# Kernel optimization log

Measured on AMD Instinct MI355X. Metric: run time of the kernel, lower is better.

## Reference

```python
import jax, jax.numpy as jnp
import numpy as np

N_HEAD = 12
HEAD_SIZE = 64
HIDDEN = N_HEAD * HEAD_SIZE  # 768


def setup_inputs() -> dict:
    key = jax.random.key(0)
    k1, k2, k3 = jax.random.split(key, 3)
    B, S = 2, 2048
    hidden_states = jax.random.normal(k1, (B, S, HIDDEN), dtype=jnp.float32)
    c_attn_w = jax.random.normal(k2, (HIDDEN, 3 * HIDDEN), dtype=jnp.float32) * 0.02
    c_attn_b = jnp.zeros((3 * HIDDEN,), dtype=jnp.float32)
    c_proj_w = jax.random.normal(k3, (HIDDEN, HIDDEN), dtype=jnp.float32) * 0.02
    c_proj_b = jnp.zeros((HIDDEN,), dtype=jnp.float32)
    return {
        "hidden_states": hidden_states,
        "c_attn_w": c_attn_w,
        "c_attn_b": c_attn_b,
        "c_proj_w": c_proj_w,
        "c_proj_b": c_proj_b,
    }


def reference(hidden_states, c_attn_w, c_attn_b, c_proj_w, c_proj_b):
    B, S, H = hidden_states.shape
    scale = 1.0 / (HEAD_SIZE ** 0.5)
    # QKV projection (Conv1D: x @ W + b)
    qkv = hidden_states @ c_attn_w + c_attn_b  # [B, S, 3H]
    q, k, v = jnp.split(qkv, 3, axis=-1)
    # [B, n_head, S, head_size]
    def split_heads(t):
        return t.reshape(B, S, N_HEAD, HEAD_SIZE).transpose(0, 2, 1, 3)
    q, k, v = split_heads(q), split_heads(k), split_heads(v)
    # scores: [B, n_head, S, S]
    scores = jnp.einsum("bhqd,bhkd->bhqk", q, k) * scale
    mask_value = jnp.finfo(hidden_states.dtype).min
    causal = jnp.triu(jnp.full((S, S), mask_value, dtype=hidden_states.dtype), k=1)
    scores = scores + causal
    weights = jax.nn.softmax(scores, axis=-1)
    ctx = jnp.einsum("bhqk,bhkd->bhqd", weights, v)  # [B, n_head, S, head_size]
    ctx = ctx.transpose(0, 2, 1, 3).reshape(B, S, H)
    out = ctx @ c_proj_w + c_proj_b
    return out
```

## Files before the change

kernel.cpp:

```cpp
#include <hip/hip_runtime.h>

typedef __bf16 bf16x8 __attribute__((ext_vector_type(8)));
typedef __bf16 bf16x4 __attribute__((ext_vector_type(4)));
typedef float  f32x4  __attribute__((ext_vector_type(4)));

#define N_HEAD 12
#define HEAD   64
#define HID    768
#define SEQ    2048
#define BATCH  2
#define BH     (BATCH*N_HEAD)
#define MROWS  (BATCH*SEQ)
#define VSTR   2080
#define SC2    0.18033688011112042f

static __device__ __forceinline__ f32x4 mfma32(bf16x8 a, bf16x8 b, f32x4 c) {
    return __builtin_amdgcn_mfma_f32_16x16x32_bf16(a, b, c, 0, 0, 0);
}

#define GLOAD_LDS16(gp, lp) __builtin_amdgcn_global_load_lds( \
    (const __attribute__((address_space(1))) void*)(gp), \
    (__attribute__((address_space(3))) void*)(lp), 16, 0, 0)

__global__ __launch_bounds__(256) void cast_f32_bf16(const float* __restrict__ in,
                                                     __bf16* __restrict__ out, int n8) {
    int i = blockIdx.x * 256 + threadIdx.x;
    if (i >= n8) return;
    const float4* p = (const float4*)in;
    float4 a = p[2*i], b = p[2*i+1];
    bf16x8 o;
    o[0]=(__bf16)a.x; o[1]=(__bf16)a.y; o[2]=(__bf16)a.z; o[3]=(__bf16)a.w;
    o[4]=(__bf16)b.x; o[5]=(__bf16)b.y; o[6]=(__bf16)b.z; o[7]=(__bf16)b.w;
    *(bf16x8*)&out[(size_t)8*i] = o;
}

__global__ __launch_bounds__(256) void transpose_cast(const float* __restrict__ in,
                                                      __bf16* __restrict__ out, int R, int C) {
    __shared__ float t[32][33];
    int bx = blockIdx.x * 32;
    int by = blockIdx.y * 32;
    int x = threadIdx.x, y = threadIdx.y;
    #pragma unroll
    for (int i = 0; i < 32; i += 8) t[y+i][x] = in[(size_t)(by+y+i)*C + bx + x];
    __syncthreads();
    #pragma unroll
    for (int i = 0; i < 32; i += 8) out[(size_t)(bx+y+i)*R + by + x] = (__bf16)t[x][y+i];
}

template<int EPI>
__global__ __launch_bounds__(256) void gemm_bt(
    const __bf16* __restrict__ A, const __bf16* __restrict__ Bt,
    const float* __restrict__ bias, float* __restrict__ Cout,
    __bf16* __restrict__ Qo, __bf16* __restrict__ Ko, __bf16* __restrict__ Vo,
    int M, int N, int K)
{
    __shared__ __align__(16) __bf16 As[128*64];
    __shared__ __align__(16) __bf16 Bs[128*64];
    int tid = threadIdx.x;
    int m0 = blockIdx.y * 128, n0 = blockIdx.x * 128;
    int wave = tid >> 6, lane = tid & 63, lr = lane & 15, lk = lane >> 4;
    int wr = wave >> 1, wc = wave & 1;

    f32x4 acc[4][4];
    f32x4 zz = {0.f, 0.f, 0.f, 0.f};
    #pragma unroll
    for (int m = 0; m < 4; m++)
        #pragma unroll
        for (int n = 0; n < 4; n++) acc[m][n] = zz;

    for (int k0 = 0; k0 < K; k0 += 64) {
        #pragma unroll
        for (int i = 0; i < 4; i++) {
            int u = tid + 256*i;
            int row = u >> 3;
            int c = (u & 7) ^ (row & 7);
            GLOAD_LDS16(&A [(size_t)(m0+row)*K + k0 + c*8], &As[(size_t)u*8]);
            GLOAD_LDS16(&Bt[(size_t)(n0+row)*K + k0 + c*8], &Bs[(size_t)u*8]);
        }
        __syncthreads();
        #pragma unroll
        for (int kk = 0; kk < 2; kk++) {
            bf16x8 af[4], bfr[4];
            #pragma unroll
            for (int m = 0; m < 4; m++) {
                int row = wr*64 + m*16 + lr;
                int byte = (row*128 + kk*64 + lk*16) ^ ((row & 7) << 4);
                af[m] = *(const bf16x8*)((const char*)As + byte);
            }
            #pragma unroll
            for (int n = 0; n < 4; n++) {
                int row = wc*64 + n*16 + lr;
                int byte = (row*128 + kk*64 + lk*16) ^ ((row & 7) << 4);
                bfr[n] = *(const bf16x8*)((const char*)Bs + byte);
            }
            #pragma unroll
            for (int m = 0; m < 4; m++)
                #pragma unroll
                for (int n = 0; n < 4; n++)
                    acc[m][n] = mfma32(af[m], bfr[n], acc[m][n]);
        }
        __syncthreads();
    }

    #pragma unroll
    for (int m = 0; m < 4; m++)
    #pragma unroll
    for (int n = 0; n < 4; n++)
    #pragma unroll
    for (int r = 0; r < 4; r++) {
        int row = m0 + wr*64 + m*16 + lk*4 + r;
        int col = n0 + wc*64 + n*16 + lr;
        float v = acc[m][n][r] + bias[col];
        if (EPI == 0) {
            Cout[(size_t)row * N + col] = v;
        } else {
            int b_idx = row >> 11, s = row & 2047;
            int which = col / HID, hc = col % HID;
            int bh = b_idx * N_HEAD + (hc >> 6);
            int d = hc & 63;
            if (which == 0)      Qo[((size_t)bh*SEQ + s)*HEAD + d] = (__bf16)(v * SC2);
            else if (which == 1) Ko[((size_t)bh*SEQ + s)*HEAD + d] = (__bf16)v;
            else                 Vo[((size_t)bh*HEAD + d)*VSTR + s] = (__bf16)v;
        }
    }
}

__global__ __launch_bounds__(256, 2) void flash_attn(
    const __bf16* __restrict__ Q, const __bf16* __restrict__ Km,
    const __bf16* __restrict__ Vt, __bf16* __restrict__ ctx)
{
    __shared__ __align__(16) __bf16 Ks[2][64*64];
    __shared__ __align__(16) __bf16 Vs[2][64*64];
    int tid = threadIdx.x;
    int w = tid >> 6;
    int lane = tid & 63;
    int lr = lane & 15, lk = lane >> 4;
    int gid = blockIdx.x;
    int bh = gid % BH;
    int qb = 15 - gid / BH;
    int b_idx = bh / N_HEAD, h = bh % N_HEAD;
    int q0 = qb*128 + w*32;
    const size_t hb = (size_t)bh * SEQ * HEAD;
    const size_t vbh = (size_t)bh * HEAD * VSTR;
    f32x4 zz = {0.f, 0.f, 0.f, 0.f};

    int u0 = tid, u1 = tid + 256;
    int kr0 = u0 >> 3, kc0 = (u0 & 7) ^ (kr0 & 7);
    int kr1 = u1 >> 3, kc1 = (u1 & 7) ^ (kr1 & 7);

    bf16x8 qf0[2], qf1[2];
    #pragma unroll
    for (int kb = 0; kb < 2; kb++) {
        qf0[kb] = *(const bf16x8*)&Q[hb + (size_t)(q0 + lr)*HEAD + kb*32 + lk*8];
        qf1[kb] = *(const bf16x8*)&Q[hb + (size_t)(q0 + 16 + lr)*HEAD + kb*32 + lk*8];
    }

    f32x4 acc0[4], acc1[4];
    float ls0 = 0.f, ls1 = 0.f;
    #pragma unroll
    for (int db = 0; db < 4; db++) { acc0[db] = zz; acc1[db] = zz; }

    int nt = 2*qb + 2;

    GLOAD_LDS16(&Km[hb + (size_t)kr0*HEAD + kc0*8],  &Ks[0][(size_t)u0*8]);
    GLOAD_LDS16(&Km[hb + (size_t)kr1*HEAD + kc1*8],  &Ks[0][(size_t)u1*8]);
    GLOAD_LDS16(&Vt[vbh + (size_t)kr0*VSTR + kc0*8], &Vs[0][(size_t)u0*8]);
    GLOAD_LDS16(&Vt[vbh + (size_t)kr1*VSTR + kc1*8], &Vs[0][(size_t)u1*8]);
    __syncthreads();

    for (int t = 0; t < nt; t++) {
        int kv0 = t * 64;
        int cur = t & 1;
        const char* kbuf = (const char*)&Ks[cur][0];
        const char* vbuf = (const char*)&Vs[cur][0];

        if (t + 1 < nt) {
            int kv1 = kv0 + 64;
            int nxt = cur ^ 1;
            GLOAD_LDS16(&Km[hb + (size_t)(kv1 + kr0)*HEAD + kc0*8],  &Ks[nxt][(size_t)u0*8]);
            GLOAD_LDS16(&Km[hb + (size_t)(kv1 + kr1)*HEAD + kc1*8],  &Ks[nxt][(size_t)u1*8]);
            GLOAD_LDS16(&Vt[vbh + (size_t)kr0*VSTR + kv1 + kc0*8],   &Vs[nxt][(size_t)u0*8]);
            GLOAD_LDS16(&Vt[vbh + (size_t)kr1*VSTR + kv1 + kc1*8],   &Vs[nxt][(size_t)u1*8]);
        }

        bf16x8 kf[4][2];
        #pragma unroll
        for (int cb = 0; cb < 4; cb++)
            #pragma unroll
            for (int kb = 0; kb < 2; kb++) {
                int row = cb*16 + lr;
                int byte = (row*128 + kb*64 + lk*16) ^ ((row & 7) << 4);
                kf[cb][kb] = *(const bf16x8*)(kbuf + byte);
            }

        bf16x8 v01[4], v23[4];
        #pragma unroll
        for (int db = 0; db < 4; db++) {
            int row = db*16 + lr;
            int rx = (row & 7) << 4;
            bf16x4 a0 = *(const bf16x4*)(vbuf + ((row*128 + lk*8)       ^ rx));
            bf16x4 a1 = *(const bf16x4*)(vbuf + ((row*128 + 32 + lk*8)  ^ rx));
            bf16x4 a2 = *(const bf16x4*)(vbuf + ((row*128 + 64 + lk*8)  ^ rx));
            bf16x4 a3 = *(const bf16x4*)(vbuf + ((row*128 + 96 + lk*8)  ^ rx));
            v01[db] = __builtin_shufflevector(a0, a1, 0,1,2,3,4,5,6,7);
            v23[db] = __builtin_shufflevector(a2, a3, 0,1,2,3,4,5,6,7);
        }

        f32x4 sc0[4], sc1[4];
        __builtin_amdgcn_s_setprio(1);
        #pragma unroll
        for (int cb = 0; cb < 4; cb++) {
            f32x4 z0 = mfma32(kf[cb][0], qf0[0], zz);
            sc0[cb] = mfma32(kf[cb][1], qf0[1], z0);
            f32x4 z1 = mfma32(kf[cb][0], qf1[0], zz);
            sc1[cb] = mfma32(kf[cb][1], qf1[1], z1);
        }
        __builtin_amdgcn_s_setprio(0);

        if (kv0 + 63 > q0) {
            #pragma unroll
            for (int cb = 0; cb < 4; cb++)
                #pragma unroll
                for (int r = 0; r < 4; r++) {
                    int kg = kv0 + cb*16 + lk*4 + r;
                    if (kg > q0 + lr)      sc0[cb][r] = -30000.f;
                    if (kg > q0 + 16 + lr) sc1[cb][r] = -30000.f;
                }
        }

        bf16x8 pa0[2], pa1[2];
        {
            float rs0 = 0.f, rs1 = 0.f;
            #pragma unroll
            for (int cb = 0; cb < 4; cb++)
                #pragma unroll
                for (int r = 0; r < 4; r++) {
                    float p0 = exp2f(sc0[cb][r]);
                    float p1 = exp2f(sc1[cb][r]);
                    rs0 += p0; rs1 += p1;
                    pa0[cb >> 1][(cb & 1)*4 + r] = (__bf16)p0;
                    pa1[cb >> 1][(cb & 1)*4 + r] = (__bf16)p1;
                }
            ls0 += rs0; ls1 += rs1;
        }

        __builtin_amdgcn_s_setprio(1);
        #pragma unroll
        for (int db = 0; db < 4; db++) {
            acc0[db] = mfma32(pa0[0], v01[db], acc0[db]);
            acc0[db] = mfma32(pa0[1], v23[db], acc0[db]);
            acc1[db] = mfma32(pa1[0], v01[db], acc1[db]);
            acc1[db] = mfma32(pa1[1], v23[db], acc1[db]);
        }
        __builtin_amdgcn_s_setprio(0);

        __syncthreads();
    }

    float rs0 = ls0;
    rs0 += __shfl_xor(rs0, 16);
    rs0 += __shfl_xor(rs0, 32);
    float rs1 = ls1;
    rs1 += __shfl_xor(rs1, 16);
    rs1 += __shfl_xor(rs1, 32);
    float rl0 = 1.0f / rs0, rl1 = 1.0f / rs1;
    float li0[4], li1[4];
    #pragma unroll
    for (int r = 0; r < 4; r++) {
        li0[r] = __shfl(rl0, (lane & 48) | (lk*4 + r));
        li1[r] = __shfl(rl1, (lane & 48) | (lk*4 + r));
    }

    #pragma unroll
    for (int db = 0; db < 4; db++)
        #pragma unroll
        for (int r = 0; r < 4; r++) {
            int d = db*16 + lr;
            int qg0 = q0 + lk*4 + r;
            int qg1 = q0 + 16 + lk*4 + r;
            ctx[((size_t)(b_idx*SEQ + qg0))*HID + h*HEAD + d] = (__bf16)(acc0[db][r] * li0[r]);
            ctx[((size_t)(b_idx*SEQ + qg1))*HID + h*HEAD + d] = (__bf16)(acc1[db][r] * li1[r]);
        }
}

extern "C" void kernel_launch(void* const* d_in, const int* in_sizes, int n_in,
                              void* d_out, int out_size, void* d_ws, size_t ws_size,
                              hipStream_t stream) {
    const float* x  = (const float*)d_in[0];
    const float* w1 = (const float*)d_in[1];
    const float* b1 = (const float*)d_in[2];
    const float* w2 = (const float*)d_in[3];
    const float* b2 = (const float*)d_in[4];
    float* out = (float*)d_out;

    char* ws = (char*)d_ws;
    size_t o = 0;
    __bf16* Xb  = (__bf16*)(ws + o); o += (size_t)MROWS*HID*2;
    __bf16* W1t = (__bf16*)(ws + o); o += (size_t)3*HID*HID*2;
    __bf16* W2t = (__bf16*)(ws + o); o += (size_t)HID*HID*2;
    __bf16* Qb  = (__bf16*)(ws + o); o += (size_t)MROWS*HID*2;
    __bf16* Kb  = (__bf16*)(ws + o); o += (size_t)MROWS*HID*2;
    __bf16* Vt  = (__bf16*)(ws + o); o += (size_t)BH*HEAD*VSTR*2;
    __bf16* CTX = (__bf16*)(ws + o); o += (size_t)MROWS*HID*2;

    cast_f32_bf16<<<(MROWS*HID/8 + 255)/256, 256, 0, stream>>>(x, Xb, MROWS*HID/8);
    transpose_cast<<<dim3(3*HID/32, HID/32), dim3(32, 8), 0, stream>>>(w1, W1t, HID, 3*HID);
    transpose_cast<<<dim3(HID/32,   HID/32), dim3(32, 8), 0, stream>>>(w2, W2t, HID, HID);

    gemm_bt<1><<<dim3(3*HID/128, MROWS/128), 256, 0, stream>>>(
        Xb, W1t, b1, nullptr, Qb, Kb, Vt, MROWS, 3*HID, HID);

    flash_attn<<<dim3(16*BH), 256, 0, stream>>>(Qb, Kb, Vt, CTX);

    gemm_bt<0><<<dim3(HID/128, MROWS/128), 256, 0, stream>>>(
        CTX, W2t, b2, out, nullptr, nullptr, nullptr, MROWS, HID, HID);
}
```

Before: 189.2 us.

## Split long causal query blocks across two KV halves and double-buffer GEMM tiles

The attention kernel now splits each of the upper eight query blocks across two workgroups that process alternating KV tiles. Each writes unnormalized partial outputs and row sums into reused workspace, and a new combine kernel merges them and normalizes. This balances the causal triangle's uneven work across more workgroups. Separately, the projection GEMM gains a double-buffered LDS prefetch of the next K tile, so loads overlap with MFMA work. The cost is an extra kernel launch, extra global traffic for the partials, and twice the GEMM LDS footprint, which may lower occupancy.

```diff
diff --git a/kernel.cpp b/kernel.cpp
--- a/kernel.cpp
+++ b/kernel.cpp
@@ -54,13 +54,21 @@
     __bf16* __restrict__ Qo, __bf16* __restrict__ Ko, __bf16* __restrict__ Vo,
     int M, int N, int K)
 {
-    __shared__ __align__(16) __bf16 As[128*64];
-    __shared__ __align__(16) __bf16 Bs[128*64];
+    __shared__ __align__(16) __bf16 As[2][128*64];
+    __shared__ __align__(16) __bf16 Bs[2][128*64];
     int tid = threadIdx.x;
     int m0 = blockIdx.y * 128, n0 = blockIdx.x * 128;
     int wave = tid >> 6, lane = tid & 63, lr = lane & 15, lk = lane >> 4;
     int wr = wave >> 1, wc = wave & 1;
 
+    int ur[4], uc[4];
+    #pragma unroll
+    for (int i = 0; i < 4; i++) {
+        int u = tid + 256*i;
+        ur[i] = u >> 3;
+        uc[i] = (u & 7) ^ (ur[i] & 7);
+    }
+
     f32x4 acc[4][4];
     f32x4 zz = {0.f, 0.f, 0.f, 0.f};
     #pragma unroll
@@ -68,16 +76,29 @@
         #pragma unroll
         for (int n = 0; n < 4; n++) acc[m][n] = zz;
 
-    for (int k0 = 0; k0 < K; k0 += 64) {
-        #pragma unroll
-        for (int i = 0; i < 4; i++) {
-            int u = tid + 256*i;
-            int row = u >> 3;
-            int c = (u & 7) ^ (row & 7);
-            GLOAD_LDS16(&A [(size_t)(m0+row)*K + k0 + c*8], &As[(size_t)u*8]);
-            GLOAD_LDS16(&Bt[(size_t)(n0+row)*K + k0 + c*8], &Bs[(size_t)u*8]);
-        }
-        __syncthreads();
+    const int NK = K >> 6;
+    #pragma unroll
+    for (int i = 0; i < 4; i++) {
+        int u = tid + 256*i;
+        GLOAD_LDS16(&A [(size_t)(m0+ur[i])*K + uc[i]*8], &As[0][(size_t)u*8]);
+        GLOAD_LDS16(&Bt[(size_t)(n0+ur[i])*K + uc[i]*8], &Bs[0][(size_t)u*8]);
+    }
+    __syncthreads();
+
+    for (int ki = 0; ki < NK; ki++) {
+        int cur = ki & 1;
+        if (ki + 1 < NK) {
+            int k1 = (ki + 1) << 6;
+            int nxt = cur ^ 1;
+            #pragma unroll
+            for (int i = 0; i < 4; i++) {
+                int u = tid + 256*i;
+                GLOAD_LDS16(&A [(size_t)(m0+ur[i])*K + k1 + uc[i]*8], &As[nxt][(size_t)u*8]);
+                GLOAD_LDS16(&Bt[(size_t)(n0+ur[i])*K + k1 + uc[i]*8], &Bs[nxt][(size_t)u*8]);
+            }
+        }
+        const char* ab = (const char*)&As[cur][0];
+        const char* bb = (const char*)&Bs[cur][0];
         #pragma unroll
         for (int kk = 0; kk < 2; kk++) {
             bf16x8 af[4], bfr[4];
@@ -85,13 +106,13 @@
             for (int m = 0; m < 4; m++) {
                 int row = wr*64 + m*16 + lr;
                 int byte = (row*128 + kk*64 + lk*16) ^ ((row & 7) << 4);
-                af[m] = *(const bf16x8*)((const char*)As + byte);
+                af[m] = *(const bf16x8*)(ab + byte);
             }
             #pragma unroll
             for (int n = 0; n < 4; n++) {
                 int row = wc*64 + n*16 + lr;
                 int byte = (row*128 + kk*64 + lk*16) ^ ((row & 7) << 4);
-                bfr[n] = *(const bf16x8*)((const char*)Bs + byte);
+                bfr[n] = *(const bf16x8*)(bb + byte);
             }
             #pragma unroll
             for (int m = 0; m < 4; m++)
@@ -127,7 +148,8 @@
 
 __global__ __launch_bounds__(256, 2) void flash_attn(
     const __bf16* __restrict__ Q, const __bf16* __restrict__ Km,
-    const __bf16* __restrict__ Vt, __bf16* __restrict__ ctx)
+    const __bf16* __restrict__ Vt, __bf16* __restrict__ ctx,
+    __bf16* __restrict__ Opart, float* __restrict__ lspart)
 {
     __shared__ __align__(16) __bf16 Ks[2][64*64];
     __shared__ __align__(16) __bf16 Vs[2][64*64];
@@ -136,8 +158,19 @@
     int lane = tid & 63;
     int lr = lane & 15, lk = lane >> 4;
     int gid = blockIdx.x;
-    int bh = gid % BH;
-    int qb = 15 - gid / BH;
+    int bh, qb, half, step;
+    if (gid < 16*BH) {
+        qb = 15 - gid / (2*BH);
+        half = (gid % (2*BH)) / BH;
+        bh = gid % BH;
+        step = 2;
+    } else {
+        int u = gid - 16*BH;
+        qb = 7 - u / BH;
+        bh = u % BH;
+        half = 0; step = 1;
+    }
+    bool split = (step == 2);
     int b_idx = bh / N_HEAD, h = bh % N_HEAD;
     int q0 = qb*128 + w*32;
     const size_t hb = (size_t)bh * SEQ * HEAD;
@@ -161,22 +194,26 @@
     for (int db = 0; db < 4; db++) { acc0[db] = zz; acc1[db] = zz; }
 
     int nt = 2*qb + 2;
-
-    GLOAD_LDS16(&Km[hb + (size_t)kr0*HEAD + kc0*8],  &Ks[0][(size_t)u0*8]);
-    GLOAD_LDS16(&Km[hb + (size_t)kr1*HEAD + kc1*8],  &Ks[0][(size_t)u1*8]);
-    GLOAD_LDS16(&Vt[vbh + (size_t)kr0*VSTR + kc0*8], &Vs[0][(size_t)u0*8]);
-    GLOAD_LDS16(&Vt[vbh + (size_t)kr1*VSTR + kc1*8], &Vs[0][(size_t)u1*8]);
+    int t0 = half;
+
+    {
+        int kv = t0 * 64;
+        GLOAD_LDS16(&Km[hb + (size_t)(kv+kr0)*HEAD + kc0*8],  &Ks[0][(size_t)u0*8]);
+        GLOAD_LDS16(&Km[hb + (size_t)(kv+kr1)*HEAD + kc1*8],  &Ks[0][(size_t)u1*8]);
+        GLOAD_LDS16(&Vt[vbh + (size_t)kr0*VSTR + kv + kc0*8], &Vs[0][(size_t)u0*8]);
+        GLOAD_LDS16(&Vt[vbh + (size_t)kr1*VSTR + kv + kc1*8], &Vs[0][(size_t)u1*8]);
+    }
     __syncthreads();
 
-    for (int t = 0; t < nt; t++) {
+    int buf = 0;
+    for (int t = t0; t < nt; t += step) {
         int kv0 = t * 64;
-        int cur = t & 1;
-        const char* kbuf = (const char*)&Ks[cur][0];
-        const char* vbuf = (const char*)&Vs[cur][0];
-
-        if (t + 1 < nt) {
-            int kv1 = kv0 + 64;
-            int nxt = cur ^ 1;
+        const char* kbuf = (const char*)&Ks[buf][0];
+        const char* vbuf = (const char*)&Vs[buf][0];
+
+        if (t + step < nt) {
+            int kv1 = (t + step) * 64;
+            int nxt = buf ^ 1;
             GLOAD_LDS16(&Km[hb + (size_t)(kv1 + kr0)*HEAD + kc0*8],  &Ks[nxt][(size_t)u0*8]);
             GLOAD_LDS16(&Km[hb + (size_t)(kv1 + kr1)*HEAD + kc1*8],  &Ks[nxt][(size_t)u1*8]);
             GLOAD_LDS16(&Vt[vbh + (size_t)kr0*VSTR + kv1 + kc0*8],   &Vs[nxt][(size_t)u0*8]);
@@ -255,6 +292,7 @@
         __builtin_amdgcn_s_setprio(0);
 
         __syncthreads();
+        buf ^= 1;
     }
 
     float rs0 = ls0;
@@ -263,6 +301,26 @@
     float rs1 = ls1;
     rs1 += __shfl_xor(rs1, 16);
     rs1 += __shfl_xor(rs1, 32);
+
+    if (split) {
+        size_t ob = ((size_t)half*BH + bh) * 1024;
+        #pragma unroll
+        for (int db = 0; db < 4; db++)
+            #pragma unroll
+            for (int r = 0; r < 4; r++) {
+                int d = db*16 + lr;
+                int qg0 = q0 + lk*4 + r;
+                int qg1 = q0 + 16 + lk*4 + r;
+                Opart[(ob + qg0 - 1024)*64 + d] = (__bf16)acc0[db][r];
+                Opart[(ob + qg1 - 1024)*64 + d] = (__bf16)acc1[db][r];
+            }
+        if (lk == 0) {
+            lspart[(size_t)half*BH*1024 + (size_t)bh*1024 + (q0 + lr - 1024)]      = rs0;
+            lspart[(size_t)half*BH*1024 + (size_t)bh*1024 + (q0 + 16 + lr - 1024)] = rs1;
+        }
+        return;
+    }
+
     float rl0 = 1.0f / rs0, rl1 = 1.0f / rs1;
     float li0[4], li1[4];
     #pragma unroll
@@ -270,7 +328,6 @@
         li0[r] = __shfl(rl0, (lane & 48) | (lk*4 + r));
         li1[r] = __shfl(rl1, (lane & 48) | (lk*4 + r));
     }
-
     #pragma unroll
     for (int db = 0; db < 4; db++)
         #pragma unroll
@@ -281,6 +338,24 @@
             ctx[((size_t)(b_idx*SEQ + qg0))*HID + h*HEAD + d] = (__bf16)(acc0[db][r] * li0[r]);
             ctx[((size_t)(b_idx*SEQ + qg1))*HID + h*HEAD + d] = (__bf16)(acc1[db][r] * li1[r]);
         }
+}
+
+__global__ __launch_bounds__(256) void combine_split(
+    const __bf16* __restrict__ Opart, const float* __restrict__ lspart,
+    __bf16* __restrict__ ctx)
+{
+    int i = blockIdx.x * 256 + threadIdx.x;
+    int row = i >> 3, dc = i & 7;
+    int bh = row >> 10, sl = row & 1023;
+    int b_idx = bh / N_HEAD, h = bh % N_HEAD;
+    bf16x8 o0 = *(const bf16x8*)&Opart[(((size_t)0*BH + bh)*1024 + sl)*64 + dc*8];
+    bf16x8 o1 = *(const bf16x8*)&Opart[(((size_t)1*BH + bh)*1024 + sl)*64 + dc*8];
+    float ls = lspart[(size_t)bh*1024 + sl] + lspart[(size_t)BH*1024 + (size_t)bh*1024 + sl];
+    float rl = 1.0f / ls;
+    bf16x8 o;
+    #pragma unroll
+    for (int j = 0; j < 8; j++) o[j] = (__bf16)(((float)o0[j] + (float)o1[j]) * rl);
+    *(bf16x8*)&ctx[((size_t)(b_idx*SEQ + 1024 + sl))*HID + h*HEAD + dc*8] = o;
 }
 
 extern "C" void kernel_launch(void* const* d_in, const int* in_sizes, int n_in,
@@ -303,6 +378,9 @@
     __bf16* Vt  = (__bf16*)(ws + o); o += (size_t)BH*HEAD*VSTR*2;
     __bf16* CTX = (__bf16*)(ws + o); o += (size_t)MROWS*HID*2;
 
+    __bf16* Opart  = Xb;
+    float*  lspart = (float*)W1t;
+
     cast_f32_bf16<<<(MROWS*HID/8 + 255)/256, 256, 0, stream>>>(x, Xb, MROWS*HID/8);
     transpose_cast<<<dim3(3*HID/32, HID/32), dim3(32, 8), 0, stream>>>(w1, W1t, HID, 3*HID);
     transpose_cast<<<dim3(HID/32,   HID/32), dim3(32, 8), 0, stream>>>(w2, W2t, HID, HID);
@@ -310,7 +388,8 @@
     gemm_bt<1><<<dim3(3*HID/128, MROWS/128), 256, 0, stream>>>(
         Xb, W1t, b1, nullptr, Qb, Kb, Vt, MROWS, 3*HID, HID);
 
-    flash_attn<<<dim3(16*BH), 256, 0, stream>>>(Qb, Kb, Vt, CTX);
+    flash_attn<<<dim3(24*BH), 256, 0, stream>>>(Qb, Kb, Vt, CTX, Opart, lspart);
+    combine_split<<<dim3(BH*1024*8/256), 256, 0, stream>>>(Opart, lspart, CTX);
 
     gemm_bt<0><<<dim3(HID/128, MROWS/128), 256, 0, stream>>>(
         CTX, W2t, b2, out, nullptr, nullptr, nullptr, MROWS, HID, HID);
```

Measured after the change: 170.1 us. -10.1%, faster.
